# Kernel tuning notes

Measured on AMD Instinct MI355X. Metric: run time of the kernel, lower is better.

## Reference

```python
import jax, jax.numpy as jnp
import numpy as np

L = 2          # lstm_layers
H = 512        # state_size
E = 512        # embedding_size
V = 512        # latent_vocab_size
T = 100        # max_dec_len
START = V - 1  # start_id
B = 128        # batch
M = 256        # mem_len
NS = 4         # num_sample


def setup_inputs() -> dict:
    key = jax.random.key(0)
    ks = jax.random.split(key, 12)
    s = 0.05
    return {
        "y": jax.random.normal(ks[0], (B, H), jnp.float32),
        "kv_emb": jax.random.normal(ks[1], (B, M, H), jnp.float32),
        "kv_mask": jnp.ones((B, M), dtype=bool),
        "z_mask": jnp.ones((B, T), jnp.float32),
        "emb": jax.random.normal(ks[2], (V, E), jnp.float32) * s,
        "W_h0": jax.random.normal(ks[3], (L * H, H), jnp.float32) * s,
        "b_h0": jnp.zeros((L * H,), jnp.float32),
        "W_c0": jax.random.normal(ks[4], (L * H, H), jnp.float32) * s,
        "b_c0": jnp.zeros((L * H,), jnp.float32),
        "W_ih": jax.random.normal(ks[5], (L, 4 * H, E), jnp.float32) * s,
        "W_hh": jax.random.normal(ks[6], (L, 4 * H, H), jnp.float32) * s,
        "b_ih": jnp.zeros((L, 4 * H), jnp.float32),
        "b_hh": jnp.zeros((L, 4 * H), jnp.float32),
        "W_attn": jax.random.normal(ks[7], (H, H), jnp.float32) * s,
        "W_cproj": jax.random.normal(ks[8], (H, 2 * H), jnp.float32) * s,
        "b_cproj": jnp.zeros((H,), jnp.float32),
        "W_out": jax.random.normal(ks[9], (V, H), jnp.float32) * s,
        "b_out": jnp.zeros((V,), jnp.float32),
        "num_sample": NS,
    }


def reference(y, kv_emb, kv_mask, z_mask, emb, W_h0, b_h0, W_c0, b_c0,
              W_ih, W_hh, b_ih, b_hh, W_attn, W_cproj, b_cproj, W_out, b_out,
              num_sample):
    n = int(num_sample)
    Bn = B * n
    # view(B,1,..).repeat(1,n,..).view(B*n,..)  ==  repeat along axis 0 (sample-minor)
    y_r = jnp.repeat(y, n, axis=0)                      # [Bn, H]
    kv_r = jnp.repeat(kv_emb, n, axis=0)                # [Bn, M, H]
    mask_add = jnp.where(jnp.repeat(kv_mask, n, axis=0), 0.0, -1e9).astype(jnp.float32)

    # init_state: project y -> per-layer h, c
    h = (y_r @ W_h0.T + b_h0).reshape(Bn, L, H).transpose(1, 0, 2)  # [L, Bn, H]
    c = (y_r @ W_c0.T + b_c0).reshape(Bn, L, H).transpose(1, 0, 2)
    x0 = emb[jnp.full((Bn,), START)]                    # start-token embedding
    base_key = jax.random.key(42)

    def step(carry, t):
        h, c, x = carry
        hs, cs = [], []
        for l in range(L):  # stacked LSTM cells (PyTorch gate order i,f,g,o)
            g = x @ W_ih[l].T + b_ih[l] + h[l] @ W_hh[l].T + b_hh[l]
            i_, f_, g_, o_ = jnp.split(g, 4, axis=-1)
            cn = jax.nn.sigmoid(f_) * c[l] + jax.nn.sigmoid(i_) * jnp.tanh(g_)
            hn = jax.nn.sigmoid(o_) * jnp.tanh(cn)
            hs.append(hn); cs.append(cn); x = hn
        out = x                                         # top-layer h, [Bn, H]
        # bilinear attention over kv memory with mask
        scores = jnp.einsum('bd,bmd->bm', out @ W_attn.T, kv_r) + mask_add
        attn = jax.nn.softmax(scores, axis=-1)
        ctx = jnp.einsum('bm,bmd->bd', attn, kv_r)
        out2 = jnp.concatenate([out, ctx], axis=-1) @ W_cproj.T + b_cproj
        logits = out2 @ W_out.T + b_out                 # output_proj
        logp = jax.nn.log_softmax(logits, axis=-1)
        # Categorical sample (strategy='unconstrained')
        idx = jax.random.categorical(jax.random.fold_in(base_key, t), logits)
        slp = jnp.take_along_axis(logp, idx[:, None], axis=-1)[:, 0]
        ent = (-jnp.exp(logp) * logp).sum(-1).mean()
        return (jnp.stack(hs), jnp.stack(cs), emb[idx]), (idx, slp, ent)

    _, (ids, slps, ents) = jax.lax.scan(step, (h, c, x0), jnp.arange(T))
    z_ids = ids.T.reshape(B, n, T)                      # [B, n, T] int
    z_states = emb[z_ids]                               # [B, n, T, E]
    stepwise = slps.T.reshape(B, n, T)
    z_lp = (stepwise * z_mask[:, None, :]).sum(-1)      # [B, n]
    ent_z = ents.mean()
    return z_ids, z_states, z_lp, stepwise, ent_z
```

## Files before the change

### kernel.cpp

```cpp
#include <hip/hip_runtime.h>
#include <hip/hip_bf16.h>

#define BATCH 128
#define NSAMP 4
#define BN    512
#define HID   512
#define EMBD  512
#define VOC   512
#define TLEN  100
#define MLEN  256
#define NGATE 2048

#define NPART 8

#define O_ZID     0L
#define O_ZSTATES 51200L
#define O_ZLP     26265600L
#define O_STEP    26266112L
#define O_ENT     26317312L
#define O_TOTAL   26317313L

#define OFF_H    0L
#define OFF_C    524288L
#define OFF_X    1048576L
#define OFF_G    1310720L
#define OFF_Q    9699328L
#define OFF_CTX  11796480L
#define OFF_O2   12058624L
#define OFF_LG   14155776L
#define OFF_YR   16252928L
#define OFF_BG   16515072L
#define OFF_ENT  16519168L
#define OFF_SLP  16519296L
#define WS_FLOATS 16570496L

#define GPSTRIDE 1048576L
#define SPSTRIDE 262144L

__device__ float g_ws[WS_FLOATS];
__device__ int   g_ids[TLEN * BN];

__device__ __forceinline__ unsigned rotl32(unsigned x, int r) {
  return (x << r) | (x >> (32 - r));
}
__device__ __forceinline__ void threefry2x32(unsigned k0, unsigned k1,
                                             unsigned& x0, unsigned& x1) {
  unsigned k2 = k0 ^ k1 ^ 0x1BD11BDAu;
#define TF_R(r) { x0 += x1; x1 = rotl32(x1, r); x1 ^= x0; }
  x0 += k0; x1 += k1;
  TF_R(13) TF_R(15) TF_R(26) TF_R(6)
  x0 += k1; x1 += k2 + 1u;
  TF_R(17) TF_R(29) TF_R(16) TF_R(24)
  x0 += k2; x1 += k0 + 2u;
  TF_R(13) TF_R(15) TF_R(26) TF_R(6)
  x0 += k0; x1 += k1 + 3u;
  TF_R(17) TF_R(29) TF_R(16) TF_R(24)
  x0 += k1; x1 += k2 + 4u;
  TF_R(13) TF_R(15) TF_R(26) TF_R(6)
  x0 += k2; x1 += k0 + 5u;
#undef TF_R
}

__device__ __forceinline__ float gumbel_from_bits(unsigned bits) {
  unsigned fb = (bits >> 9) | 0x3F800000u;
  float f = __uint_as_float(fb) - 1.0f;
  const float TINY = 1.17549435e-38f;
  float u = fmaxf(f + TINY, TINY);
  return -logf(-logf(u));
}

__device__ __forceinline__ float sigf(float x) {
  return 0.5f + 0.5f * tanhf(0.5f * x);
}

__device__ __forceinline__ float4 add4(float4 a, float4 b) {
  a.x += b.x; a.y += b.y; a.z += b.z; a.w += b.w; return a;
}

__global__ __launch_bounds__(64) void gemmsk(
    long offA1, int lda1, int P1, long strideP1,
    const float* __restrict__ B1, int ldb1, int K1,
    long offA2, int lda2,
    const float* __restrict__ B2, int ldb2,
    const float* __restrict__ biasExt, long biasOff,
    long offC, int ldc, int Kc)
{
  __shared__ float As[16][64];
  __shared__ float Bs[16][64];
  const int t  = threadIdx.x;
  const int tm = t >> 3;
  const int tn = t & 7;
  const int m0 = blockIdx.y * 64;
  const int n0 = blockIdx.x * 64;
  const int kp = blockIdx.z;

  int kbase = kp * Kc;
  const float* A; const float* B; int lda, ldb, P; long strideP;
  if (kbase < K1) {
    A = g_ws + offA1; B = B1; lda = lda1; ldb = ldb1; P = P1; strideP = strideP1;
  } else {
    A = g_ws + offA2; B = B2; lda = lda2; ldb = ldb2; P = 1; strideP = 0;
    kbase -= K1;
  }

  float acc[8][8];
#pragma unroll
  for (int i = 0; i < 8; ++i)
#pragma unroll
    for (int j = 0; j < 8; ++j) acc[i][j] = 0.f;

  for (int k0 = 0; k0 < Kc; k0 += 16) {
    const int kg = kbase + k0;
    const float* pa = A + (size_t)(m0 + t) * lda + kg;
    float4 a0, a1, a2, a3;
    {
      const float4* q4 = (const float4*)pa;
      a0 = q4[0]; a1 = q4[1]; a2 = q4[2]; a3 = q4[3];
      for (int p = 1; p < P; ++p) {
        const float4* r4 = (const float4*)(pa + (size_t)p * strideP);
        a0 = add4(a0, r4[0]); a1 = add4(a1, r4[1]);
        a2 = add4(a2, r4[2]); a3 = add4(a3, r4[3]);
      }
    }
    const float4* pb = (const float4*)(B + (size_t)(n0 + t) * ldb + kg);
    float4 b0 = pb[0], b1 = pb[1], b2 = pb[2], b3 = pb[3];

    __syncthreads();
    As[ 0][t] = a0.x; As[ 1][t] = a0.y; As[ 2][t] = a0.z; As[ 3][t] = a0.w;
    As[ 4][t] = a1.x; As[ 5][t] = a1.y; As[ 6][t] = a1.z; As[ 7][t] = a1.w;
    As[ 8][t] = a2.x; As[ 9][t] = a2.y; As[10][t] = a2.z; As[11][t] = a2.w;
    As[12][t] = a3.x; As[13][t] = a3.y; As[14][t] = a3.z; As[15][t] = a3.w;
    Bs[ 0][t] = b0.x; Bs[ 1][t] = b0.y; Bs[ 2][t] = b0.z; Bs[ 3][t] = b0.w;
    Bs[ 4][t] = b1.x; Bs[ 5][t] = b1.y; Bs[ 6][t] = b1.z; Bs[ 7][t] = b1.w;
    Bs[ 8][t] = b2.x; Bs[ 9][t] = b2.y; Bs[10][t] = b2.z; Bs[11][t] = b2.w;
    Bs[12][t] = b3.x; Bs[13][t] = b3.y; Bs[14][t] = b3.z; Bs[15][t] = b3.w;
    __syncthreads();

#pragma unroll
    for (int k = 0; k < 16; ++k) {
      float av[8], bv[8];
      *(float4*)&av[0] = *(const float4*)&As[k][tm * 8];
      *(float4*)&av[4] = *(const float4*)&As[k][tm * 8 + 4];
      *(float4*)&bv[0] = *(const float4*)&Bs[k][tn * 8];
      *(float4*)&bv[4] = *(const float4*)&Bs[k][tn * 8 + 4];
#pragma unroll
      for (int i = 0; i < 8; ++i)
#pragma unroll
        for (int j = 0; j < 8; ++j)
          acc[i][j] += av[i] * bv[j];
    }
  }

  const int Mtot = gridDim.y * 64;
  float* C = g_ws + offC + (size_t)kp * (size_t)Mtot * ldc;
  const float* bias = nullptr;
  if (kp == 0)
    bias = biasExt ? biasExt : (biasOff >= 0 ? g_ws + biasOff : nullptr);
#pragma unroll
  for (int i = 0; i < 8; ++i) {
    const int row = m0 + tm * 8 + i;
    const int col = n0 + tn * 8;
    float4 o0, o1;
    o0.x = acc[i][0]; o0.y = acc[i][1]; o0.z = acc[i][2]; o0.w = acc[i][3];
    o1.x = acc[i][4]; o1.y = acc[i][5]; o1.z = acc[i][6]; o1.w = acc[i][7];
    if (bias) {
      o0.x += bias[col];     o0.y += bias[col + 1];
      o0.z += bias[col + 2]; o0.w += bias[col + 3];
      o1.x += bias[col + 4]; o1.y += bias[col + 5];
      o1.z += bias[col + 6]; o1.w += bias[col + 7];
    }
    *(float4*)(C + (size_t)row * ldc + col)     = o0;
    *(float4*)(C + (size_t)row * ldc + col + 4) = o1;
  }
}

__global__ __launch_bounds__(256) void gemm2(
    long offA1, int lda1,
    const float* __restrict__ B1, int ldb1, int K1,
    long offA2, int lda2,
    const float* __restrict__ B2, int ldb2, int K2,
    const float* __restrict__ biasExt, long biasOff,
    long offC, int ldc)
{
  __shared__ float As[16][68];
  __shared__ float Bs[16][68];
  const int tid = threadIdx.x;
  const int tx  = tid & 15;
  const int ty  = tid >> 4;
  const int ldr = tid >> 2;
  const int ldk = (tid & 3) << 2;
  const int m0 = blockIdx.y * 64;
  const int n0 = blockIdx.x * 64;
  float acc[4][4] = {{0.f}};

  for (int seg = 0; seg < 2; ++seg) {
    const float* A = g_ws + (seg ? offA2 : offA1);
    const float* B = seg ? B2 : B1;
    const int lda = seg ? lda2 : lda1;
    const int ldb = seg ? ldb2 : ldb1;
    const int K   = seg ? K2  : K1;
    for (int k0 = 0; k0 < K; k0 += 16) {
      float4 av = *(const float4*)(A + (size_t)(m0 + ldr) * lda + k0 + ldk);
      float4 bv = *(const float4*)(B + (size_t)(n0 + ldr) * ldb + k0 + ldk);
      __syncthreads();
      As[ldk + 0][ldr] = av.x; As[ldk + 1][ldr] = av.y;
      As[ldk + 2][ldr] = av.z; As[ldk + 3][ldr] = av.w;
      Bs[ldk + 0][ldr] = bv.x; Bs[ldk + 1][ldr] = bv.y;
      Bs[ldk + 2][ldr] = bv.z; Bs[ldk + 3][ldr] = bv.w;
      __syncthreads();
#pragma unroll
      for (int k = 0; k < 16; ++k) {
        float4 a = *(const float4*)&As[k][ty * 4];
        float4 b = *(const float4*)&Bs[k][tx * 4];
        acc[0][0] += a.x * b.x; acc[0][1] += a.x * b.y; acc[0][2] += a.x * b.z; acc[0][3] += a.x * b.w;
        acc[1][0] += a.y * b.x; acc[1][1] += a.y * b.y; acc[1][2] += a.y * b.z; acc[1][3] += a.y * b.w;
        acc[2][0] += a.z * b.x; acc[2][1] += a.z * b.y; acc[2][2] += a.z * b.z; acc[2][3] += a.z * b.w;
        acc[3][0] += a.w * b.x; acc[3][1] += a.w * b.y; acc[3][2] += a.w * b.z; acc[3][3] += a.w * b.w;
      }
    }
  }
  const float* bias = biasExt ? biasExt : (biasOff >= 0 ? g_ws + biasOff : nullptr);
  float* C = g_ws + offC;
#pragma unroll
  for (int i = 0; i < 4; ++i) {
    int row = m0 + ty * 4 + i;
    int col = n0 + tx * 4;
    float4 o;
    o.x = acc[i][0]; o.y = acc[i][1]; o.z = acc[i][2]; o.w = acc[i][3];
    if (bias) {
      o.x += bias[col]; o.y += bias[col + 1]; o.z += bias[col + 2]; o.w += bias[col + 3];
    }
    *(float4*)(C + (size_t)row * ldc + col) = o;
  }
}

__global__ __launch_bounds__(256) void lstm_cell(long hoff, long coff)
{
  int idx = blockIdx.x * 256 + threadIdx.x;
  int r = idx >> 9, j = idx & 511;
  float gi = 0.f, gf = 0.f, gg = 0.f, go = 0.f;
  const size_t rb = (size_t)r * NGATE;
#pragma unroll
  for (int p = 0; p < NPART; ++p) {
    const float* gr = g_ws + OFF_G + (size_t)p * GPSTRIDE + rb;
    gi += gr[j]; gf += gr[512 + j]; gg += gr[1024 + j]; go += gr[1536 + j];
  }
  float* h = g_ws + hoff;
  float* c = g_ws + coff;
  float cold = c[(size_t)r * 1024 + j];
  float cn = sigf(gf) * cold + sigf(gi) * tanhf(gg);
  float hn = sigf(go) * tanhf(cn);
  c[(size_t)r * 1024 + j] = cn;
  h[(size_t)r * 1024 + j] = hn;
}

__global__ __launch_bounds__(256) void attn_kernel(
    const float* __restrict__ kv,
    const void*  __restrict__ kvm_raw)
{
  __shared__ float qs[4][512];
  __shared__ float sc[4][256];
  const int b = blockIdx.x;
  const int tid = threadIdx.x;
  const int lane = tid & 63, wave = tid >> 6;
  float* ctx = g_ws + OFF_CTX;
  const float* kvb = kv + (size_t)b * MLEN * HID;
  const unsigned* w32 = (const unsigned*)kvm_raw;
  const unsigned char* u8 = (const unsigned char*)kvm_raw;
  const bool u8mode = (w32[0] == 0x01010101u);
#pragma unroll
  for (int s = 0; s < 4; ++s) {
    float q0 = 0.f, q1 = 0.f;
    const size_t base = (size_t)(b * 4 + s) * HID + tid;
#pragma unroll
    for (int p = 0; p < NPART; ++p) {
      q0 += g_ws[OFF_Q + (size_t)p * SPSTRIDE + base];
      q1 += g_ws[OFF_Q + (size_t)p * SPSTRIDE + base + 256];
    }
    qs[s][tid] = q0; qs[s][tid + 256] = q1;
  }
  __syncthreads();
  for (int m = wave; m < MLEN; m += 4) {
    const float* kr = kvb + (size_t)m * HID;
    float a0 = 0.f, a1 = 0.f, a2 = 0.f, a3 = 0.f;
    for (int d = lane; d < HID; d += 64) {
      float kvv = kr[d];
      a0 += qs[0][d] * kvv; a1 += qs[1][d] * kvv;
      a2 += qs[2][d] * kvv; a3 += qs[3][d] * kvv;
    }
#pragma unroll
    for (int off = 32; off > 0; off >>= 1) {
      a0 += __shfl_down(a0, off); a1 += __shfl_down(a1, off);
      a2 += __shfl_down(a2, off); a3 += __shfl_down(a3, off);
    }
    if (lane == 0) {
      bool on = u8mode ? (u8[b * MLEN + m] != 0) : (w32[b * MLEN + m] != 0u);
      float madd = on ? 0.0f : -1e9f;
      sc[0][m] = a0 + madd; sc[1][m] = a1 + madd;
      sc[2][m] = a2 + madd; sc[3][m] = a3 + madd;
    }
  }
  __syncthreads();
  {
    const int s = wave;
    float mx = -3.4e38f;
    for (int m = lane; m < MLEN; m += 64) mx = fmaxf(mx, sc[s][m]);
#pragma unroll
    for (int off = 32; off > 0; off >>= 1) mx = fmaxf(mx, __shfl_xor(mx, off));
    float sum = 0.f;
    for (int m = lane; m < MLEN; m += 64) {
      float e = expf(sc[s][m] - mx);
      sc[s][m] = e; sum += e;
    }
#pragma unroll
    for (int off = 32; off > 0; off >>= 1) sum += __shfl_xor(sum, off);
    for (int m = lane; m < MLEN; m += 64) sc[s][m] = sc[s][m] / sum;
  }
  __syncthreads();
  float c00=0,c01=0,c10=0,c11=0,c20=0,c21=0,c30=0,c31=0;
  for (int m = 0; m < MLEN; ++m) {
    float k0v = kvb[(size_t)m * HID + tid];
    float k1v = kvb[(size_t)m * HID + tid + 256];
    float p0 = sc[0][m], p1 = sc[1][m], p2 = sc[2][m], p3 = sc[3][m];
    c00 += p0 * k0v; c01 += p0 * k1v;
    c10 += p1 * k0v; c11 += p1 * k1v;
    c20 += p2 * k0v; c21 += p2 * k1v;
    c30 += p3 * k0v; c31 += p3 * k1v;
  }
  ctx[(size_t)(b * 4 + 0) * HID + tid] = c00; ctx[(size_t)(b * 4 + 0) * HID + tid + 256] = c01;
  ctx[(size_t)(b * 4 + 1) * HID + tid] = c10; ctx[(size_t)(b * 4 + 1) * HID + tid + 256] = c11;
  ctx[(size_t)(b * 4 + 2) * HID + tid] = c20; ctx[(size_t)(b * 4 + 2) * HID + tid + 256] = c21;
  ctx[(size_t)(b * 4 + 3) * HID + tid] = c30; ctx[(size_t)(b * 4 + 3) * HID + tid + 256] = c31;
}

__global__ __launch_bounds__(256) void sample_step(
    const float* __restrict__ emb, int t)
{
  __shared__ float rz[256];
  __shared__ int   ri[256];
  __shared__ float rl[256];
  const int row = blockIdx.x;
  const int tid = threadIdx.x;
  float* xbuf = g_ws + OFF_X;

  unsigned fk0 = 0u, fk1 = (unsigned)t;
  threefry2x32(0u, 42u, fk0, fk1);

  float l[2], g[2];
#pragma unroll
  for (int j = 0; j < 2; ++j) {
    int v = tid + j * 256;
    unsigned c0 = 0u, c1 = (unsigned)(row * VOC + v);
    threefry2x32(fk0, fk1, c0, c1);
    g[j] = gumbel_from_bits(c0 ^ c1);
    float lv = 0.f;
    const size_t base = (size_t)row * VOC + v;
#pragma unroll
    for (int p = 0; p < NPART; ++p)
      lv += g_ws[OFF_LG + (size_t)p * SPSTRIDE + base];
    l[j] = lv;
  }

  float z0 = l[0] + g[0], z1 = l[1] + g[1];
  float bz; int bi; float bl;
  if (z1 > z0) { bz = z1; bi = tid + 256; bl = l[1]; }
  else         { bz = z0; bi = tid;       bl = l[0]; }
  rz[tid] = bz; ri[tid] = bi; rl[tid] = bl;
  __syncthreads();
  for (int s = 128; s > 0; s >>= 1) {
    if (tid < s) {
      float oz = rz[tid + s]; int oi = ri[tid + s];
      if (oz > rz[tid] || (oz == rz[tid] && oi < ri[tid])) {
        rz[tid] = oz; ri[tid] = oi; rl[tid] = rl[tid + s];
      }
    }
    __syncthreads();
  }
  const int idx = ri[0];
  const float l_at = rl[0];
  __syncthreads();

  rz[tid] = fmaxf(l[0], l[1]);
  __syncthreads();
  for (int s = 128; s > 0; s >>= 1) {
    if (tid < s) rz[tid] = fmaxf(rz[tid], rz[tid + s]);
    __syncthreads();
  }
  const float m = rz[0];
  __syncthreads();

  float d0 = l[0] - m, d1 = l[1] - m;
  float e0 = expf(d0), e1 = expf(d1);
  rz[tid] = e0 + e1;
  rl[tid] = e0 * d0 + e1 * d1;
  __syncthreads();
  for (int s = 128; s > 0; s >>= 1) {
    if (tid < s) { rz[tid] += rz[tid + s]; rl[tid] += rl[tid + s]; }
    __syncthreads();
  }
  if (tid == 0) {
    float S = rz[0], W = rl[0];
    float logS = logf(S);
    g_ids[t * BN + row] = idx;
    g_ws[OFF_SLP + t * BN + row] = (l_at - m) - logS;
    atomicAdd(&g_ws[OFF_ENT + t], logS - W / S);
  }
  const float* er = emb + (size_t)idx * EMBD;
  xbuf[(size_t)row * EMBD + tid]       = er[tid];
  xbuf[(size_t)row * EMBD + tid + 256] = er[tid + 256];
}

__global__ __launch_bounds__(256) void init_misc(
    const float* __restrict__ y, const float* __restrict__ emb,
    const float* __restrict__ b_ih, const float* __restrict__ b_hh)
{
  int gid = blockIdx.x * 256 + threadIdx.x;
  int r = gid >> 9, col = gid & 511;
  g_ws[OFF_YR + gid] = y[(size_t)(r >> 2) * HID + col];
  g_ws[OFF_X + gid]  = emb[(size_t)(VOC - 1) * EMBD + col];
  if (gid < 2 * NGATE) g_ws[OFF_BG + gid] = b_ih[gid] + b_hh[gid];
  if (gid < 128) g_ws[OFF_ENT + gid] = 0.0f;
}

__global__ __launch_bounds__(256) void write_out(
    const float* __restrict__ emb, const float* __restrict__ zmask,
    float* __restrict__ out)
{
  long i = (long)blockIdx.x * 256 + threadIdx.x;
  const long stride = (long)gridDim.x * 256;
  for (; i < O_TOTAL; i += stride) {
    float v;
    if (i < O_ZSTATES) {
      int bs = (int)(i / TLEN), t = (int)(i % TLEN);
      v = (float)g_ids[t * BN + bs];
    } else if (i < O_ZLP) {
      long j = i - O_ZSTATES;
      int e = (int)(j & 511);
      int bst = (int)(j >> 9);
      int bs = bst / TLEN, t = bst % TLEN;
      v = emb[(size_t)g_ids[t * BN + bs] * EMBD + e];
    } else if (i < O_STEP) {
      int bs = (int)(i - O_ZLP);
      int b = bs >> 2;
      float acc = 0.f;
      for (int t = 0; t < TLEN; ++t)
        acc += g_ws[OFF_SLP + t * BN + bs] * zmask[b * TLEN + t];
      v = acc;
    } else if (i < O_ENT) {
      long j = i - O_STEP;
      int bs = (int)(j / TLEN), t = (int)(j % TLEN);
      v = g_ws[OFF_SLP + t * BN + bs];
    } else {
      float e = 0.f;
      for (int t = 0; t < TLEN; ++t) e += g_ws[OFF_ENT + t];
      v = e / (float)(BN * TLEN);
    }
    out[i] = v;
  }
}

extern "C" void kernel_launch(void* const* d_in, const int* in_sizes, int n_in,
                              void* d_out, int out_size, void* d_ws, size_t ws_size,
                              hipStream_t stream) {
  (void)in_sizes; (void)n_in; (void)out_size; (void)d_ws; (void)ws_size;
  const float* y       = (const float*)d_in[0];
  const float* kv      = (const float*)d_in[1];
  const void*  kvm     = (const void*)d_in[2];
  const float* zmask   = (const float*)d_in[3];
  const float* emb     = (const float*)d_in[4];
  const float* W_h0    = (const float*)d_in[5];
  const float* b_h0    = (const float*)d_in[6];
  const float* W_c0    = (const float*)d_in[7];
  const float* b_c0    = (const float*)d_in[8];
  const float* W_ih    = (const float*)d_in[9];
  const float* W_hh    = (const float*)d_in[10];
  const float* b_ih    = (const float*)d_in[11];
  const float* b_hh    = (const float*)d_in[12];
  const float* W_attn  = (const float*)d_in[13];
  const float* W_cproj = (const float*)d_in[14];
  const float* b_cproj = (const float*)d_in[15];
  const float* W_out   = (const float*)d_in[16];
  const float* b_out   = (const float*)d_in[17];
  float* out = (float*)d_out;

  init_misc<<<1024, 256, 0, stream>>>(y, emb, b_ih, b_hh);

  dim3 g_init(1024 / 64, 512 / 64);
  gemm2<<<g_init, 256, 0, stream>>>(OFF_YR, 512, W_h0, 512, 512,
                                    0L, 0, nullptr, 0, 0, b_h0, -1L, OFF_H, 1024);
  gemm2<<<g_init, 256, 0, stream>>>(OFF_YR, 512, W_c0, 512, 512,
                                    0L, 0, nullptr, 0, 0, b_c0, -1L, OFF_C, 1024);

  dim3 g_gates(2048 / 64, 512 / 64, NPART);
  dim3 g_sq(512 / 64, 512 / 64, NPART);
  const size_t WL = (size_t)NGATE * HID;

  for (int t = 0; t < TLEN; ++t) {
    gemmsk<<<g_gates, 64, 0, stream>>>(OFF_X, 512, 1, 0L, W_ih, 512, 512,
                                       OFF_H, 1024, W_hh, 512,
                                       nullptr, OFF_BG, OFF_G, NGATE, 128);
    lstm_cell<<<1024, 256, 0, stream>>>(OFF_H, OFF_C);
    gemmsk<<<g_gates, 64, 0, stream>>>(OFF_H, 1024, 1, 0L, W_ih + WL, 512, 512,
                                       OFF_H + 512, 1024, W_hh + WL, 512,
                                       nullptr, OFF_BG + NGATE, OFF_G, NGATE, 128);
    lstm_cell<<<1024, 256, 0, stream>>>(OFF_H + 512, OFF_C + 512);
    gemmsk<<<g_sq, 64, 0, stream>>>(OFF_H + 512, 1024, 1, 0L, W_attn, 512, 512,
                                    0L, 0, nullptr, 0,
                                    nullptr, -1L, OFF_Q, 512, 64);
    attn_kernel<<<128, 256, 0, stream>>>(kv, kvm);
    gemmsk<<<g_sq, 64, 0, stream>>>(OFF_H + 512, 1024, 1, 0L, W_cproj, 1024, 512,
                                    OFF_CTX, 512, W_cproj + 512, 1024,
                                    b_cproj, -1L, OFF_O2, 512, 128);
    gemmsk<<<g_sq, 64, 0, stream>>>(OFF_O2, 512, NPART, SPSTRIDE, W_out, 512, 512,
                                    0L, 0, nullptr, 0,
                                    b_out, -1L, OFF_LG, 512, 64);
    sample_step<<<512, 256, 0, stream>>>(emb, t);
  }

  int wblocks = (int)((O_TOTAL + 255L) / 256L);
  write_out<<<wblocks, 256, 0, stream>>>(emb, zmask, out);
}
```

Baseline: 23.29 ms.

## Fuse layer-2 cell, attention, projections and sampling into two per-batch kernels

Each decode step's layer-2 LSTM cell, query projection, attention, context projection, output projection and sampling are merged into two kernels with one 512-thread block per batch item. Each block holds its 4 sample rows in shared memory. This removes four launches per step and the split-K partial buffers written to and read back from global memory. In exchange only 128 blocks run, and every block streams the full W_attn, W_cproj and W_out matrices with per-thread row reads that are not coalesced, which may cost more bandwidth than the launches saved.

```diff
diff --git a/kernel.cpp b/kernel.cpp
--- a/kernel.cpp
+++ b/kernel.cpp
@@ -1,5 +1,4 @@
 #include <hip/hip_runtime.h>
-#include <hip/hip_bf16.h>
 
 #define BATCH 128
 #define NSAMP 4
@@ -24,10 +23,7 @@
 #define OFF_C    524288L
 #define OFF_X    1048576L
 #define OFF_G    1310720L
-#define OFF_Q    9699328L
-#define OFF_CTX  11796480L
 #define OFF_O2   12058624L
-#define OFF_LG   14155776L
 #define OFF_YR   16252928L
 #define OFF_BG   16515072L
 #define OFF_ENT  16519168L
@@ -35,7 +31,6 @@
 #define WS_FLOATS 16570496L
 
 #define GPSTRIDE 1048576L
-#define SPSTRIDE 262144L
 
 __device__ float g_ws[WS_FLOATS];
 __device__ int   g_ids[TLEN * BN];
@@ -254,160 +249,247 @@
   h[(size_t)r * 1024 + j] = hn;
 }
 
-__global__ __launch_bounds__(256) void attn_kernel(
-    const float* __restrict__ kv,
-    const void*  __restrict__ kvm_raw)
-{
+__global__ __launch_bounds__(512) void attn_mega(
+    const float* __restrict__ kv, const void* __restrict__ kvm_raw,
+    const float* __restrict__ W_attn, const float* __restrict__ W_cproj,
+    const float* __restrict__ b_cproj)
+{
+  __shared__ float h1s[4][512];
   __shared__ float qs[4][512];
-  __shared__ float sc[4][256];
+  __shared__ float scb[4][256];
+  __shared__ float ctxs[4][512];
   const int b = blockIdx.x;
   const int tid = threadIdx.x;
-  const int lane = tid & 63, wave = tid >> 6;
-  float* ctx = g_ws + OFF_CTX;
-  const float* kvb = kv + (size_t)b * MLEN * HID;
-  const unsigned* w32 = (const unsigned*)kvm_raw;
-  const unsigned char* u8 = (const unsigned char*)kvm_raw;
-  const bool u8mode = (w32[0] == 0x01010101u);
-#pragma unroll
-  for (int s = 0; s < 4; ++s) {
-    float q0 = 0.f, q1 = 0.f;
-    const size_t base = (size_t)(b * 4 + s) * HID + tid;
+  const int lane = tid & 63, wv = tid >> 6;
+
+  for (int e = tid; e < 2048; e += 512) {
+    const int s = e >> 9, j = e & 511;
+    const int row = b * 4 + s;
+    float gi = 0.f, gf = 0.f, gg = 0.f, go = 0.f;
+    const size_t rb = (size_t)row * NGATE;
 #pragma unroll
     for (int p = 0; p < NPART; ++p) {
-      q0 += g_ws[OFF_Q + (size_t)p * SPSTRIDE + base];
-      q1 += g_ws[OFF_Q + (size_t)p * SPSTRIDE + base + 256];
-    }
-    qs[s][tid] = q0; qs[s][tid + 256] = q1;
-  }
-  __syncthreads();
-  for (int m = wave; m < MLEN; m += 4) {
-    const float* kr = kvb + (size_t)m * HID;
-    float a0 = 0.f, a1 = 0.f, a2 = 0.f, a3 = 0.f;
-    for (int d = lane; d < HID; d += 64) {
-      float kvv = kr[d];
-      a0 += qs[0][d] * kvv; a1 += qs[1][d] * kvv;
-      a2 += qs[2][d] * kvv; a3 += qs[3][d] * kvv;
-    }
-#pragma unroll
-    for (int off = 32; off > 0; off >>= 1) {
-      a0 += __shfl_down(a0, off); a1 += __shfl_down(a1, off);
-      a2 += __shfl_down(a2, off); a3 += __shfl_down(a3, off);
-    }
-    if (lane == 0) {
-      bool on = u8mode ? (u8[b * MLEN + m] != 0) : (w32[b * MLEN + m] != 0u);
-      float madd = on ? 0.0f : -1e9f;
-      sc[0][m] = a0 + madd; sc[1][m] = a1 + madd;
-      sc[2][m] = a2 + madd; sc[3][m] = a3 + madd;
-    }
-  }
-  __syncthreads();
+      const float* gr = g_ws + OFF_G + (size_t)p * GPSTRIDE + rb;
+      gi += gr[j]; gf += gr[512 + j]; gg += gr[1024 + j]; go += gr[1536 + j];
+    }
+    float* h = g_ws + OFF_H + 512;
+    float* c = g_ws + OFF_C + 512;
+    float cold = c[(size_t)row * 1024 + j];
+    float cn = sigf(gf) * cold + sigf(gi) * tanhf(gg);
+    float hn = sigf(go) * tanhf(cn);
+    c[(size_t)row * 1024 + j] = cn;
+    h[(size_t)row * 1024 + j] = hn;
+    h1s[s][j] = hn;
+  }
+  __syncthreads();
+
   {
-    const int s = wave;
+    const int d = tid;
+    const float* wr = W_attn + (size_t)d * 512;
+    float t0 = 0.f, t1 = 0.f, t2 = 0.f, t3 = 0.f;
+#pragma unroll 1
+    for (int p = 0; p < 8; ++p) {
+      float a0 = 0.f, a1 = 0.f, a2 = 0.f, a3 = 0.f;
+      const int k0 = p * 64;
+      for (int k = 0; k < 64; ++k) {
+        const float w = wr[k0 + k];
+        a0 += h1s[0][k0 + k] * w; a1 += h1s[1][k0 + k] * w;
+        a2 += h1s[2][k0 + k] * w; a3 += h1s[3][k0 + k] * w;
+      }
+      t0 += a0; t1 += a1; t2 += a2; t3 += a3;
+    }
+    qs[0][d] = t0; qs[1][d] = t1; qs[2][d] = t2; qs[3][d] = t3;
+  }
+  __syncthreads();
+
+  {
+    const float* kvb = kv + (size_t)b * MLEN * HID;
+    const unsigned* w32 = (const unsigned*)kvm_raw;
+    const unsigned char* u8 = (const unsigned char*)kvm_raw;
+    const bool u8mode = (w32[0] == 0x01010101u);
+    for (int m = wv; m < MLEN; m += 8) {
+      const float* kr = kvb + (size_t)m * HID;
+      float a0 = 0.f, a1 = 0.f, a2 = 0.f, a3 = 0.f;
+      for (int d = lane; d < HID; d += 64) {
+        float kvv = kr[d];
+        a0 += qs[0][d] * kvv; a1 += qs[1][d] * kvv;
+        a2 += qs[2][d] * kvv; a3 += qs[3][d] * kvv;
+      }
+#pragma unroll
+      for (int off = 32; off > 0; off >>= 1) {
+        a0 += __shfl_down(a0, off); a1 += __shfl_down(a1, off);
+        a2 += __shfl_down(a2, off); a3 += __shfl_down(a3, off);
+      }
+      if (lane == 0) {
+        bool on = u8mode ? (u8[b * MLEN + m] != 0) : (w32[b * MLEN + m] != 0u);
+        float madd = on ? 0.0f : -1e9f;
+        scb[0][m] = a0 + madd; scb[1][m] = a1 + madd;
+        scb[2][m] = a2 + madd; scb[3][m] = a3 + madd;
+      }
+    }
+  }
+  __syncthreads();
+
+  if (wv < 4) {
+    const int s = wv;
     float mx = -3.4e38f;
-    for (int m = lane; m < MLEN; m += 64) mx = fmaxf(mx, sc[s][m]);
+    for (int m = lane; m < MLEN; m += 64) mx = fmaxf(mx, scb[s][m]);
 #pragma unroll
     for (int off = 32; off > 0; off >>= 1) mx = fmaxf(mx, __shfl_xor(mx, off));
     float sum = 0.f;
     for (int m = lane; m < MLEN; m += 64) {
-      float e = expf(sc[s][m] - mx);
-      sc[s][m] = e; sum += e;
+      float e = expf(scb[s][m] - mx);
+      scb[s][m] = e; sum += e;
     }
 #pragma unroll
     for (int off = 32; off > 0; off >>= 1) sum += __shfl_xor(sum, off);
-    for (int m = lane; m < MLEN; m += 64) sc[s][m] = sc[s][m] / sum;
-  }
-  __syncthreads();
-  float c00=0,c01=0,c10=0,c11=0,c20=0,c21=0,c30=0,c31=0;
-  for (int m = 0; m < MLEN; ++m) {
-    float k0v = kvb[(size_t)m * HID + tid];
-    float k1v = kvb[(size_t)m * HID + tid + 256];
-    float p0 = sc[0][m], p1 = sc[1][m], p2 = sc[2][m], p3 = sc[3][m];
-    c00 += p0 * k0v; c01 += p0 * k1v;
-    c10 += p1 * k0v; c11 += p1 * k1v;
-    c20 += p2 * k0v; c21 += p2 * k1v;
-    c30 += p3 * k0v; c31 += p3 * k1v;
-  }
-  ctx[(size_t)(b * 4 + 0) * HID + tid] = c00; ctx[(size_t)(b * 4 + 0) * HID + tid + 256] = c01;
-  ctx[(size_t)(b * 4 + 1) * HID + tid] = c10; ctx[(size_t)(b * 4 + 1) * HID + tid + 256] = c11;
-  ctx[(size_t)(b * 4 + 2) * HID + tid] = c20; ctx[(size_t)(b * 4 + 2) * HID + tid + 256] = c21;
-  ctx[(size_t)(b * 4 + 3) * HID + tid] = c30; ctx[(size_t)(b * 4 + 3) * HID + tid + 256] = c31;
-}
-
-__global__ __launch_bounds__(256) void sample_step(
-    const float* __restrict__ emb, int t)
-{
-  __shared__ float rz[256];
-  __shared__ int   ri[256];
-  __shared__ float rl[256];
-  const int row = blockIdx.x;
+    for (int m = lane; m < MLEN; m += 64) scb[s][m] = scb[s][m] / sum;
+  }
+  __syncthreads();
+
+  {
+    const float* kvb = kv + (size_t)b * MLEN * HID;
+    float c0 = 0.f, c1 = 0.f, c2 = 0.f, c3 = 0.f;
+    for (int m = 0; m < MLEN; ++m) {
+      float kvv = kvb[(size_t)m * HID + tid];
+      c0 += scb[0][m] * kvv; c1 += scb[1][m] * kvv;
+      c2 += scb[2][m] * kvv; c3 += scb[3][m] * kvv;
+    }
+    ctxs[0][tid] = c0; ctxs[1][tid] = c1; ctxs[2][tid] = c2; ctxs[3][tid] = c3;
+  }
+  __syncthreads();
+
+  {
+    const int n = tid;
+    const float* wr = W_cproj + (size_t)n * 1024;
+    const float bn = b_cproj[n];
+    float t0 = 0.f, t1 = 0.f, t2 = 0.f, t3 = 0.f;
+#pragma unroll 1
+    for (int p = 0; p < 8; ++p) {
+      float a0 = 0.f, a1 = 0.f, a2 = 0.f, a3 = 0.f;
+      const int kb = p * 128;
+      if (p < 4) {
+        for (int k = 0; k < 128; ++k) {
+          const float w = wr[kb + k];
+          a0 += h1s[0][kb + k] * w; a1 += h1s[1][kb + k] * w;
+          a2 += h1s[2][kb + k] * w; a3 += h1s[3][kb + k] * w;
+        }
+      } else {
+        const int cb = kb - 512;
+        for (int k = 0; k < 128; ++k) {
+          const float w = wr[kb + k];
+          a0 += ctxs[0][cb + k] * w; a1 += ctxs[1][cb + k] * w;
+          a2 += ctxs[2][cb + k] * w; a3 += ctxs[3][cb + k] * w;
+        }
+      }
+      if (p == 0) {
+        t0 = a0 + bn; t1 = a1 + bn; t2 = a2 + bn; t3 = a3 + bn;
+      } else {
+        t0 += a0; t1 += a1; t2 += a2; t3 += a3;
+      }
+    }
+    float* o2 = g_ws + OFF_O2;
+    o2[(size_t)(b * 4 + 0) * 512 + n] = t0;
+    o2[(size_t)(b * 4 + 1) * 512 + n] = t1;
+    o2[(size_t)(b * 4 + 2) * 512 + n] = t2;
+    o2[(size_t)(b * 4 + 3) * 512 + n] = t3;
+  }
+}
+
+__global__ __launch_bounds__(512) void sample_mega(
+    const float* __restrict__ emb, const float* __restrict__ W_out,
+    const float* __restrict__ b_out, int t)
+{
+  __shared__ float o2s[4][512];
+  __shared__ float lgs[4][512];
+  const int b = blockIdx.x;
   const int tid = threadIdx.x;
-  float* xbuf = g_ws + OFF_X;
-
-  unsigned fk0 = 0u, fk1 = (unsigned)t;
-  threefry2x32(0u, 42u, fk0, fk1);
-
-  float l[2], g[2];
-#pragma unroll
-  for (int j = 0; j < 2; ++j) {
-    int v = tid + j * 256;
-    unsigned c0 = 0u, c1 = (unsigned)(row * VOC + v);
-    threefry2x32(fk0, fk1, c0, c1);
-    g[j] = gumbel_from_bits(c0 ^ c1);
-    float lv = 0.f;
-    const size_t base = (size_t)row * VOC + v;
-#pragma unroll
-    for (int p = 0; p < NPART; ++p)
-      lv += g_ws[OFF_LG + (size_t)p * SPSTRIDE + base];
-    l[j] = lv;
-  }
-
-  float z0 = l[0] + g[0], z1 = l[1] + g[1];
-  float bz; int bi; float bl;
-  if (z1 > z0) { bz = z1; bi = tid + 256; bl = l[1]; }
-  else         { bz = z0; bi = tid;       bl = l[0]; }
-  rz[tid] = bz; ri[tid] = bi; rl[tid] = bl;
-  __syncthreads();
-  for (int s = 128; s > 0; s >>= 1) {
-    if (tid < s) {
-      float oz = rz[tid + s]; int oi = ri[tid + s];
-      if (oz > rz[tid] || (oz == rz[tid] && oi < ri[tid])) {
-        rz[tid] = oz; ri[tid] = oi; rl[tid] = rl[tid + s];
-      }
-    }
-    __syncthreads();
-  }
-  const int idx = ri[0];
-  const float l_at = rl[0];
-  __syncthreads();
-
-  rz[tid] = fmaxf(l[0], l[1]);
-  __syncthreads();
-  for (int s = 128; s > 0; s >>= 1) {
-    if (tid < s) rz[tid] = fmaxf(rz[tid], rz[tid + s]);
-    __syncthreads();
-  }
-  const float m = rz[0];
-  __syncthreads();
-
-  float d0 = l[0] - m, d1 = l[1] - m;
-  float e0 = expf(d0), e1 = expf(d1);
-  rz[tid] = e0 + e1;
-  rl[tid] = e0 * d0 + e1 * d1;
-  __syncthreads();
-  for (int s = 128; s > 0; s >>= 1) {
-    if (tid < s) { rz[tid] += rz[tid + s]; rl[tid] += rl[tid + s]; }
-    __syncthreads();
-  }
-  if (tid == 0) {
-    float S = rz[0], W = rl[0];
-    float logS = logf(S);
-    g_ids[t * BN + row] = idx;
-    g_ws[OFF_SLP + t * BN + row] = (l_at - m) - logS;
-    atomicAdd(&g_ws[OFF_ENT + t], logS - W / S);
-  }
-  const float* er = emb + (size_t)idx * EMBD;
-  xbuf[(size_t)row * EMBD + tid]       = er[tid];
-  xbuf[(size_t)row * EMBD + tid + 256] = er[tid + 256];
+  const int lane = tid & 63, wv = tid >> 6;
+
+  for (int e = tid; e < 2048; e += 512) {
+    const int s = e >> 9, j = e & 511;
+    o2s[s][j] = g_ws[OFF_O2 + (size_t)(b * 4 + s) * 512 + j];
+  }
+  __syncthreads();
+
+  {
+    const int v = tid;
+    const float* wr = W_out + (size_t)v * 512;
+    const float bv = b_out[v];
+    float t0 = 0.f, t1 = 0.f, t2 = 0.f, t3 = 0.f;
+#pragma unroll 1
+    for (int p = 0; p < 8; ++p) {
+      float a0 = 0.f, a1 = 0.f, a2 = 0.f, a3 = 0.f;
+      const int k0 = p * 64;
+      for (int k = 0; k < 64; ++k) {
+        const float w = wr[k0 + k];
+        a0 += o2s[0][k0 + k] * w; a1 += o2s[1][k0 + k] * w;
+        a2 += o2s[2][k0 + k] * w; a3 += o2s[3][k0 + k] * w;
+      }
+      if (p == 0) { t0 = a0 + bv; t1 = a1 + bv; t2 = a2 + bv; t3 = a3 + bv; }
+      else        { t0 += a0; t1 += a1; t2 += a2; t3 += a3; }
+    }
+    lgs[0][v] = t0; lgs[1][v] = t1; lgs[2][v] = t2; lgs[3][v] = t3;
+  }
+  __syncthreads();
+
+  if (wv < 4) {
+    const int row = b * 4 + wv;
+    unsigned fk0 = 0u, fk1 = (unsigned)t;
+    threefry2x32(0u, 42u, fk0, fk1);
+
+    float m = -3.4e38f;
+#pragma unroll
+    for (int j = 0; j < 8; ++j) m = fmaxf(m, lgs[wv][lane + j * 64]);
+#pragma unroll
+    for (int off = 32; off > 0; off >>= 1) m = fmaxf(m, __shfl_xor(m, off));
+
+    float bz = -3.4e38f; int bi = VOC;
+#pragma unroll
+    for (int j = 0; j < 8; ++j) {
+      const int v = lane + j * 64;
+      unsigned c0 = 0u, c1 = (unsigned)(row * VOC + v);
+      threefry2x32(fk0, fk1, c0, c1);
+      float z = lgs[wv][v] + gumbel_from_bits(c0 ^ c1);
+      if (z > bz || (z == bz && v < bi)) { bz = z; bi = v; }
+    }
+#pragma unroll
+    for (int off = 32; off > 0; off >>= 1) {
+      float oz = __shfl_xor(bz, off); int oi = __shfl_xor(bi, off);
+      if (oz > bz || (oz == bz && oi < bi)) { bz = oz; bi = oi; }
+    }
+    const int idx = bi;
+
+    float e0  = expf(lgs[wv][lane      ] - m), e1 = expf(lgs[wv][lane + 256] - m);
+    float e2  = expf(lgs[wv][lane + 128] - m), e3 = expf(lgs[wv][lane + 384] - m);
+    float e4  = expf(lgs[wv][lane +  64] - m), e5 = expf(lgs[wv][lane + 320] - m);
+    float e6  = expf(lgs[wv][lane + 192] - m), e7 = expf(lgs[wv][lane + 448] - m);
+    float d0  = lgs[wv][lane      ] - m, d1 = lgs[wv][lane + 256] - m;
+    float d2  = lgs[wv][lane + 128] - m, d3 = lgs[wv][lane + 384] - m;
+    float d4  = lgs[wv][lane +  64] - m, d5 = lgs[wv][lane + 320] - m;
+    float d6  = lgs[wv][lane + 192] - m, d7 = lgs[wv][lane + 448] - m;
+    float S = ((e0 + e1) + (e2 + e3)) + ((e4 + e5) + (e6 + e7));
+    float W = ((e0 * d0 + e1 * d1) + (e2 * d2 + e3 * d3))
+            + ((e4 * d4 + e5 * d5) + (e6 * d6 + e7 * d7));
+#pragma unroll
+    for (int off = 32; off > 0; off >>= 1) {
+      S += __shfl_down(S, off);
+      W += __shfl_down(W, off);
+    }
+
+    if (lane == 0) {
+      const float l_at = lgs[wv][idx];
+      const float logS = logf(S);
+      g_ids[t * BN + row] = idx;
+      g_ws[OFF_SLP + t * BN + row] = (l_at - m) - logS;
+      atomicAdd(&g_ws[OFF_ENT + t], logS - W / S);
+    }
+
+    float* xbuf = g_ws + OFF_X;
+    const float* er = emb + (size_t)idx * EMBD;
+    *(float4*)&xbuf[(size_t)row * EMBD + lane * 8]     = *(const float4*)&er[lane * 8];
+    *(float4*)&xbuf[(size_t)row * EMBD + lane * 8 + 4] = *(const float4*)&er[lane * 8 + 4];
+  }
 }
 
 __global__ __launch_bounds__(256) void init_misc(
@@ -492,7 +574,6 @@
                                     0L, 0, nullptr, 0, 0, b_c0, -1L, OFF_C, 1024);
 
   dim3 g_gates(2048 / 64, 512 / 64, NPART);
-  dim3 g_sq(512 / 64, 512 / 64, NPART);
   const size_t WL = (size_t)NGATE * HID;
 
   for (int t = 0; t < TLEN; ++t) {
@@ -503,18 +584,8 @@
     gemmsk<<<g_gates, 64, 0, stream>>>(OFF_H, 1024, 1, 0L, W_ih + WL, 512, 512,
                                        OFF_H + 512, 1024, W_hh + WL, 512,
                                        nullptr, OFF_BG + NGATE, OFF_G, NGATE, 128);
-    lstm_cell<<<1024, 256, 0, stream>>>(OFF_H + 512, OFF_C + 512);
-    gemmsk<<<g_sq, 64, 0, stream>>>(OFF_H + 512, 1024, 1, 0L, W_attn, 512, 512,
-                                    0L, 0, nullptr, 0,
-                                    nullptr, -1L, OFF_Q, 512, 64);
-    attn_kernel<<<128, 256, 0, stream>>>(kv, kvm);
-    gemmsk<<<g_sq, 64, 0, stream>>>(OFF_H + 512, 1024, 1, 0L, W_cproj, 1024, 512,
-                                    OFF_CTX, 512, W_cproj + 512, 1024,
-                                    b_cproj, -1L, OFF_O2, 512, 128);
-    gemmsk<<<g_sq, 64, 0, stream>>>(OFF_O2, 512, NPART, SPSTRIDE, W_out, 512, 512,
-                                    0L, 0, nullptr, 0,
-                                    b_out, -1L, OFF_LG, 512, 64);
-    sample_step<<<512, 256, 0, stream>>>(emb, t);
+    attn_mega<<<128, 512, 0, stream>>>(kv, kvm, W_attn, W_cproj, b_cproj);
+    sample_mega<<<128, 512, 0, stream>>>(emb, W_out, b_out, t);
   }
 
   int wblocks = (int)((O_TOTAL + 255L) / 256L);
```

After: 25.39 ms. 9.0% more time.

## Fuse split-K gate GEMM partials into one block and pre-reduce O2 partials

Applied to the files above, without the earlier changes.

Replaces the 8-way split-K gate GEMM, which wrote partial sums to global memory for lstm_cell to add up, with a 512-thread kernel. Each wave in it computes one K-slice of a 64x64 tile with an 8x8 register micro-tile, and the slices are reduced through shared memory before bias is added and the result is stored once. lstm_cell then reads a single gate value instead of eight partials. A separate o2_reduce kernel collapses the cproj split-K partials once, so the W_out GEMM no longer re-sums them per tile. This costs an extra launch per step and uses heavier registers and LDS per block, which lowers occupancy (only 256 blocks for the gate GEMM).

```diff
diff --git a/kernel.cpp b/kernel.cpp
--- a/kernel.cpp
+++ b/kernel.cpp
@@ -1,5 +1,4 @@
 #include <hip/hip_runtime.h>
-#include <hip/hip_bf16.h>
 
 #define BATCH 128
 #define NSAMP 4
@@ -32,9 +31,9 @@
 #define OFF_BG   16515072L
 #define OFF_ENT  16519168L
 #define OFF_SLP  16519296L
-#define WS_FLOATS 16570496L
-
-#define GPSTRIDE 1048576L
+#define OFF_O2R  16570496L
+#define WS_FLOATS 16832640L
+
 #define SPSTRIDE 262144L
 
 __device__ float g_ws[WS_FLOATS];
@@ -77,6 +76,88 @@
   a.x += b.x; a.y += b.y; a.z += b.z; a.w += b.w; return a;
 }
 
+__global__ __launch_bounds__(512) void gates_fused(
+    long offA1, int lda1, const float* __restrict__ B1, int K1,
+    long offA2, int lda2, const float* __restrict__ B2,
+    long biasOff, long offC)
+{
+  __shared__ float S[16384];
+  const int tid  = threadIdx.x;
+  const int w    = tid >> 6;
+  const int lane = tid & 63;
+  const int tm = lane >> 3, tn = lane & 7;
+  const int m0 = blockIdx.y * 64;
+  const int n0 = blockIdx.x * 64;
+  float* As = S + w * 2048;
+  float* Bs = As + 1024;
+
+  int kbase = w * 128;
+  const float* A; const float* B; int lda;
+  if (kbase < K1) { A = g_ws + offA1; lda = lda1; B = B1; }
+  else            { A = g_ws + offA2; lda = lda2; B = B2; kbase -= K1; }
+
+  float acc[8][8];
+#pragma unroll
+  for (int i = 0; i < 8; ++i)
+#pragma unroll
+    for (int j = 0; j < 8; ++j) acc[i][j] = 0.f;
+
+  for (int k0 = 0; k0 < 128; k0 += 16) {
+    const int kg = kbase + k0;
+    const float4* q4 = (const float4*)(A + (size_t)(m0 + lane) * lda + kg);
+    float4 a0 = q4[0], a1 = q4[1], a2 = q4[2], a3 = q4[3];
+    const float4* pb = (const float4*)(B + (size_t)(n0 + lane) * 512 + kg);
+    float4 b0 = pb[0], b1 = pb[1], b2 = pb[2], b3 = pb[3];
+
+    __syncthreads();
+    As[ 0*64+lane]=a0.x; As[ 1*64+lane]=a0.y; As[ 2*64+lane]=a0.z; As[ 3*64+lane]=a0.w;
+    As[ 4*64+lane]=a1.x; As[ 5*64+lane]=a1.y; As[ 6*64+lane]=a1.z; As[ 7*64+lane]=a1.w;
+    As[ 8*64+lane]=a2.x; As[ 9*64+lane]=a2.y; As[10*64+lane]=a2.z; As[11*64+lane]=a2.w;
+    As[12*64+lane]=a3.x; As[13*64+lane]=a3.y; As[14*64+lane]=a3.z; As[15*64+lane]=a3.w;
+    Bs[ 0*64+lane]=b0.x; Bs[ 1*64+lane]=b0.y; Bs[ 2*64+lane]=b0.z; Bs[ 3*64+lane]=b0.w;
+    Bs[ 4*64+lane]=b1.x; Bs[ 5*64+lane]=b1.y; Bs[ 6*64+lane]=b1.z; Bs[ 7*64+lane]=b1.w;
+    Bs[ 8*64+lane]=b2.x; Bs[ 9*64+lane]=b2.y; Bs[10*64+lane]=b2.z; Bs[11*64+lane]=b2.w;
+    Bs[12*64+lane]=b3.x; Bs[13*64+lane]=b3.y; Bs[14*64+lane]=b3.z; Bs[15*64+lane]=b3.w;
+    __syncthreads();
+
+#pragma unroll
+    for (int k = 0; k < 16; ++k) {
+      float av[8], bv[8];
+      *(float4*)&av[0] = *(const float4*)&As[k*64 + tm*8];
+      *(float4*)&av[4] = *(const float4*)&As[k*64 + tm*8 + 4];
+      *(float4*)&bv[0] = *(const float4*)&Bs[k*64 + tn*8];
+      *(float4*)&bv[4] = *(const float4*)&Bs[k*64 + tn*8 + 4];
+#pragma unroll
+      for (int i = 0; i < 8; ++i)
+#pragma unroll
+        for (int j = 0; j < 8; ++j)
+          acc[i][j] += av[i] * bv[j];
+    }
+  }
+
+  const float* bias = g_ws + biasOff;
+  float* red = S;
+  for (int s = 0; s < 4; ++s) {
+    __syncthreads();
+    if ((tm >> 1) == s) {
+      const int rb = (tm & 1) * 8;
+#pragma unroll
+      for (int i = 0; i < 8; ++i)
+#pragma unroll
+        for (int j = 0; j < 8; ++j)
+          red[w * 1024 + (rb + i) * 64 + tn * 8 + j] = acc[i][j];
+    }
+    __syncthreads();
+    for (int u = tid; u < 1024; u += 512) {
+      const int r = u >> 6, c = u & 63;
+      float t = red[u] + bias[n0 + c];
+#pragma unroll
+      for (int p = 1; p < 8; ++p) t += red[p * 1024 + u];
+      g_ws[offC + (size_t)(m0 + s * 16 + r) * 2048 + n0 + c] = t;
+    }
+  }
+}
+
 __global__ __launch_bounds__(64) void gemmsk(
     long offA1, int lda1, int P1, long strideP1,
     const float* __restrict__ B1, int ldb1, int K1,
@@ -238,13 +319,8 @@
 {
   int idx = blockIdx.x * 256 + threadIdx.x;
   int r = idx >> 9, j = idx & 511;
-  float gi = 0.f, gf = 0.f, gg = 0.f, go = 0.f;
-  const size_t rb = (size_t)r * NGATE;
-#pragma unroll
-  for (int p = 0; p < NPART; ++p) {
-    const float* gr = g_ws + OFF_G + (size_t)p * GPSTRIDE + rb;
-    gi += gr[j]; gf += gr[512 + j]; gg += gr[1024 + j]; go += gr[1536 + j];
-  }
+  const float* gr = g_ws + OFF_G + (size_t)r * NGATE;
+  float gi = gr[j], gf = gr[512 + j], gg = gr[1024 + j], go = gr[1536 + j];
   float* h = g_ws + hoff;
   float* c = g_ws + coff;
   float cold = c[(size_t)r * 1024 + j];
@@ -252,6 +328,15 @@
   float hn = sigf(go) * tanhf(cn);
   c[(size_t)r * 1024 + j] = cn;
   h[(size_t)r * 1024 + j] = hn;
+}
+
+__global__ __launch_bounds__(256) void o2_reduce()
+{
+  int e = blockIdx.x * 256 + threadIdx.x;
+  float t = g_ws[OFF_O2 + e];
+#pragma unroll
+  for (int p = 1; p < 8; ++p) t += g_ws[OFF_O2 + (size_t)p * SPSTRIDE + e];
+  g_ws[OFF_O2R + e] = t;
 }
 
 __global__ __launch_bounds__(256) void attn_kernel(
@@ -491,18 +576,18 @@
   gemm2<<<g_init, 256, 0, stream>>>(OFF_YR, 512, W_c0, 512, 512,
                                     0L, 0, nullptr, 0, 0, b_c0, -1L, OFF_C, 1024);
 
-  dim3 g_gates(2048 / 64, 512 / 64, NPART);
+  dim3 g_gf(2048 / 64, 512 / 64);
   dim3 g_sq(512 / 64, 512 / 64, NPART);
   const size_t WL = (size_t)NGATE * HID;
 
   for (int t = 0; t < TLEN; ++t) {
-    gemmsk<<<g_gates, 64, 0, stream>>>(OFF_X, 512, 1, 0L, W_ih, 512, 512,
-                                       OFF_H, 1024, W_hh, 512,
-                                       nullptr, OFF_BG, OFF_G, NGATE, 128);
+    gates_fused<<<g_gf, 512, 0, stream>>>(OFF_X, 512, W_ih, 512,
+                                          OFF_H, 1024, W_hh,
+                                          OFF_BG, OFF_G);
     lstm_cell<<<1024, 256, 0, stream>>>(OFF_H, OFF_C);
-    gemmsk<<<g_gates, 64, 0, stream>>>(OFF_H, 1024, 1, 0L, W_ih + WL, 512, 512,
-                                       OFF_H + 512, 1024, W_hh + WL, 512,
-                                       nullptr, OFF_BG + NGATE, OFF_G, NGATE, 128);
+    gates_fused<<<g_gf, 512, 0, stream>>>(OFF_H, 1024, W_ih + WL, 512,
+                                          OFF_H + 512, 1024, W_hh + WL,
+                                          OFF_BG + NGATE, OFF_G);
     lstm_cell<<<1024, 256, 0, stream>>>(OFF_H + 512, OFF_C + 512);
     gemmsk<<<g_sq, 64, 0, stream>>>(OFF_H + 512, 1024, 1, 0L, W_attn, 512, 512,
                                     0L, 0, nullptr, 0,
@@ -511,7 +596,8 @@
     gemmsk<<<g_sq, 64, 0, stream>>>(OFF_H + 512, 1024, 1, 0L, W_cproj, 1024, 512,
                                     OFF_CTX, 512, W_cproj + 512, 1024,
                                     b_cproj, -1L, OFF_O2, 512, 128);
-    gemmsk<<<g_sq, 64, 0, stream>>>(OFF_O2, 512, NPART, SPSTRIDE, W_out, 512, 512,
+    o2_reduce<<<1024, 256, 0, stream>>>();
+    gemmsk<<<g_sq, 64, 0, stream>>>(OFF_O2R, 512, 1, 0L, W_out, 512, 512,
                                     0L, 0, nullptr, 0,
                                     b_out, -1L, OFF_LG, 512, 64);
     sample_step<<<512, 256, 0, stream>>>(emb, t);
```

Result: faster. 21.45 ms (-7.9%).
